# Kernel optimization log

Hardware: AMD Instinct MI355X
Metric: run time of the kernel (lower is better)

## Reference

```python
import jax, jax.numpy as jnp
import numpy as np

N, E = 100000, 3200000
F_NODE, F_EDGE = 2, 7
H, C = 4, 8
HC = H * C
REG, TGT = 500, 1
NUM_LAYERS = 3
ATT_SLOPE = 0.2   # LeakyReLU inside GATv2 attention
ACT_SLOPE = 0.01  # model-level LeakyReLU default
BN_EPS = 1e-5


def gatv2(x, src, dst, e_attr, Wl, bl, Wr, br, We, att, bias):
    n = x.shape[0]
    xl = (x @ Wl + bl).reshape(n, H, C)          # source transform (messages)
    xr = (x @ Wr + br).reshape(n, H, C)          # destination transform
    ee = (e_attr @ We).reshape(-1, H, C)         # edge transform (no bias in PyG)
    m = jax.nn.leaky_relu(xl[src] + xr[dst] + ee, ATT_SLOPE)  # [Ef,H,C]
    logits = jnp.einsum('ehc,hc->eh', m, att)    # [Ef,H]
    mx = jax.ops.segment_max(logits, dst, num_segments=n)
    ex = jnp.exp(logits - mx[dst])
    den = jax.ops.segment_sum(ex, dst, num_segments=n)
    alpha = ex / (den[dst] + 1e-16)              # edge-softmax grouped by dst
    out = jax.ops.segment_sum(xl[src] * alpha[:, :, None], dst, num_segments=n)
    return out.reshape(n, HC) + bias             # concat heads + bias


def setup_inputs() -> dict:
    key = jax.random.key(0)
    ks = jax.random.split(key, 30)
    # edges with no self loops (module calls add_self_loops on top)
    s = jax.random.randint(ks[0], (E,), 0, N, dtype=jnp.int32)
    off = jax.random.randint(ks[1], (E,), 1, N, dtype=jnp.int32)
    d = (s + off) % N
    edge_index = jnp.stack([s, d])
    x = jax.random.normal(ks[2], (N, F_NODE), dtype=jnp.float32)
    edge_attr = jax.random.normal(ks[3], (E, F_EDGE), dtype=jnp.float32)

    def glorot(k, shape):
        fan = shape[0] + shape[-1]
        return jax.random.normal(k, shape, dtype=jnp.float32) * jnp.sqrt(2.0 / fan)

    inp = dict(x=x, edge_index=edge_index, edge_attr=edge_attr)
    i = 4
    for tag, fin in (("1", F_NODE), ("2", HC)):
        inp["Wl" + tag] = glorot(ks[i], (fin, HC)); i += 1
        inp["bl" + tag] = jnp.zeros((HC,), jnp.float32)
        inp["Wr" + tag] = glorot(ks[i], (fin, HC)); i += 1
        inp["br" + tag] = jnp.zeros((HC,), jnp.float32)
        inp["We" + tag] = glorot(ks[i], (F_EDGE, HC)); i += 1
        inp["att" + tag] = glorot(ks[i], (H, C)); i += 1
        inp["b" + tag] = jnp.zeros((HC,), jnp.float32)
    inp["gamma"] = jnp.ones((HC,), jnp.float32)
    inp["beta"] = jnp.zeros((HC,), jnp.float32)
    inp["Wreg"] = glorot(ks[i], (HC, REG)); i += 1
    inp["breg"] = jnp.zeros((REG,), jnp.float32)
    inp["Wend"] = glorot(ks[i], (REG, TGT)); i += 1
    inp["bend"] = jnp.zeros((TGT,), jnp.float32)
    return inp


def reference(x, edge_index, edge_attr,
              Wl1, bl1, Wr1, br1, We1, att1, b1,
              Wl2, bl2, Wr2, br2, We2, att2, b2,
              gamma, beta, Wreg, breg, Wend, bend):
    n = x.shape[0]
    loop = jnp.arange(n, dtype=edge_index.dtype)
    srcf = jnp.concatenate([edge_index[0], loop])
    dstf = jnp.concatenate([edge_index[1], loop])
    # self-loop edge attrs filled with mean (PyG fill_value='mean')
    ea_mean = jnp.mean(edge_attr, axis=0, keepdims=True)
    eaf = jnp.concatenate([edge_attr, jnp.broadcast_to(ea_mean, (n, edge_attr.shape[1]))])

    h = gatv2(x, srcf, dstf, eaf, Wl1, bl1, Wr1, br1, We1, att1, b1)
    for _ in range(NUM_LAYERS - 1):
        mu = jnp.mean(h, axis=0)
        var = jnp.var(h, axis=0)
        h = (h - mu) * jax.lax.rsqrt(var + BN_EPS) * gamma + beta
        h = jax.nn.leaky_relu(h, ACT_SLOPE)
        h = gatv2(h, srcf, dstf, eaf, Wl2, bl2, Wr2, br2, We2, att2, b2)
    h = jax.nn.leaky_relu(h, ACT_SLOPE)
    h = h @ Wreg + breg
    return h @ Wend + bend
```

## Files before the change

### kernel.cpp

```cpp
#include <hip/hip_runtime.h>
#include <hip/hip_fp16.h>
#include <math.h>

#define NN 100000
#define EE 3200000
#define FE 7
#define GNB 32
#define CRR 1280
#define NBK 391
#define BKCAP 8688
#define T1 4096
#define FB1 ((EE + T1 - 1) / T1)

typedef unsigned int uivec4 __attribute__((ext_vector_type(4)));
static __device__ __forceinline__ uint4 ntload4(const uint4* p) {
    uivec4 v = __builtin_nontemporal_load((const uivec4*)p);
    uint4 r; r.x = v.x; r.y = v.y; r.z = v.z; r.w = v.w; return r;
}

static __device__ __forceinline__ __half2 hmax2(__half2 a, __half2 b) {
    unsigned int ua = *(unsigned int*)&a, ub = *(unsigned int*)&b, ur;
    asm("v_pk_max_f16 %0, %1, %2" : "=v"(ur) : "v"(ua), "v"(ub));
    return *(__half2*)&ur;
}


__global__ void k_prep(const float* __restrict__ Wreg, const float* __restrict__ breg,
                       const float* __restrict__ Wend, const float* __restrict__ bend,
                       float* __restrict__ wend, float* __restrict__ c0v,
                       int* __restrict__ gbucket) {
    if (blockIdx.x == 0) {
        int t = threadIdx.x;
        if (t < 32) {
            float s = 0.f;
            for (int k = 0; k < 500; ++k) s = fmaf(Wreg[t * 500 + k], Wend[k], s);
            wend[t] = s;
        } else if (t == 32) {
            float s = 0.f;
            for (int k = 0; k < 500; ++k) s = fmaf(breg[k], Wend[k], s);
            *c0v = s + bend[0];
        }
    } else {
        for (int i = threadIdx.x; i < NBK; i += 256) gbucket[i] = i * BKCAP;
    }
}

__global__ __launch_bounds__(512) void k_fill1(const int* __restrict__ ei,
                                               const float* __restrict__ ea,
                                               int* __restrict__ gbucket,
                                               uint4* __restrict__ srt,
                                               double* __restrict__ ea_sum) {
    __shared__ int hbin[NBK];
    __shared__ float part[8][FE];
    for (int i = threadIdx.x; i < NBK; i += 512) hbin[i] = 0;
    __syncthreads();
    int e0 = blockIdx.x * T1;
    int rb[8];
#pragma unroll
    for (int i = 0; i < 8; ++i) {
        int e = e0 + i * 512 + threadIdx.x;
        int v = -1;
        if (e < EE) {
            int d = __builtin_nontemporal_load(ei + EE + e);
            int b = d >> 8;
            int r = atomicAdd(&hbin[b], 1);
            v = (r << 17) | ((d & 255) << 9) | b;
        }
        rb[i] = v;
    }
    __syncthreads();
    for (int i = threadIdx.x; i < NBK; i += 512) {
        int c = hbin[i];
        hbin[i] = (c > 0) ? atomicAdd(&gbucket[i], c) : 0;
    }
    __syncthreads();
    float acc[FE];
#pragma unroll
    for (int f = 0; f < FE; ++f) acc[f] = 0.f;
#pragma unroll
    for (int i = 0; i < 8; ++i) {
        int v = rb[i];
        if (v < 0) continue;
        int e = e0 + i * 512 + threadIdx.x;
        int b = v & 511;
        unsigned dl = (unsigned)((v >> 9) & 255);
        int r = v >> 17;
        int pos = hbin[b] + r;
        int s = __builtin_nontemporal_load(ei + e);
        const float* rr = ea + (size_t)e * FE;
        unsigned h[FE];
#pragma unroll
        for (int f = 0; f < FE; ++f) {
            float af = __builtin_nontemporal_load(rr + f);
            acc[f] += af;
            h[f] = (unsigned)__half_as_ushort(__float2half_rn(af));
        }
#pragma unroll
        for (int f = 0; f < 6; ++f) { h[f] = (h[f] + 1) >> 1; if (h[f] > 0x7FFFu) h[f] = 0x7FFFu; }
        unsigned h6 = (h[6] + 4) >> 3; if (h6 > 0x1FFFu) h6 = 0x1FFFu;
        uint4 u;
        u.x = h[0] | (h[1] << 15) | ((dl & 3u) << 30);
        u.y = h[2] | (h[3] << 15) | (((dl >> 2) & 3u) << 30);
        u.z = h[4] | (h[5] << 15) | (((dl >> 4) & 3u) << 30);
        u.w = (unsigned)s | (h6 << 17) | ((dl >> 6) << 30);
        srt[(size_t)pos] = u;
    }
    int wave = threadIdx.x >> 6;
#pragma unroll
    for (int f = 0; f < FE; ++f) {
        float v = acc[f];
        for (int o = 32; o > 0; o >>= 1) v += __shfl_down(v, o, 64);
        if ((threadIdx.x & 63) == 0) part[wave][f] = v;
    }
    __syncthreads();
    if (threadIdx.x < FE) {
        float s = 0.f;
#pragma unroll
        for (int i = 0; i < 8; ++i) s += part[i][threadIdx.x];
        atomicAdd(&ea_sum[threadIdx.x], (double)s);
    }
}

__global__ __launch_bounds__(512) void k_bscan(const int* __restrict__ gbucket,
                                               int* __restrict__ bbase,
                                               const double* __restrict__ ea_sum,
                                               float* __restrict__ ea_mean) {
    __shared__ int ts[512];
    int t = threadIdx.x;
    if (t < 8) ea_mean[t] = (t < FE) ? (float)(ea_sum[t] / (double)EE) : 0.f;
    int c = (t < NBK) ? (gbucket[t] - t * BKCAP) : 0;
    ts[t] = c;
    __syncthreads();
    for (int o = 1; o < 512; o <<= 1) {
        int u = (t >= o) ? ts[t - o] : 0;
        __syncthreads();
        ts[t] += u;
        __syncthreads();
    }
    if (t < NBK) bbase[t] = ts[t] - c;
}

__global__ __launch_bounds__(512) void k_fill2(const uint4* __restrict__ srt,
                                               const int* __restrict__ gbucket,
                                               const int* __restrict__ bbase,
                                               int* __restrict__ offs,
                                               uint4* __restrict__ rec) {
    __shared__ int hist[256], hcopy[256], strt[256];
    int t = threadIdx.x;
    int b = blockIdx.x;
    int nbase = b << 8;
    int nb = NN - nbase; if (nb > 256) nb = 256;
    int sbase = b * BKCAP;
    int cnt = gbucket[b] - sbase;
    int bb = bbase[b];
    if (t < 256) hist[t] = 0;
    __syncthreads();
    for (int p = t; p < cnt; p += 512) {
        uint4 s = srt[(size_t)(sbase + p)];
        int dl = (int)((s.x >> 30) | ((s.y >> 30) << 2) | ((s.z >> 30) << 4) | ((s.w >> 30) << 6));
        atomicAdd(&hist[dl], 1);
    }
    __syncthreads();
    if (t < 256) hcopy[t] = hist[t];
    __syncthreads();
    for (int o = 1; o < 256; o <<= 1) {
        int u = 0;
        if (t < 256 && t >= o) u = hist[t - o];
        __syncthreads();
        if (t < 256) hist[t] += u;
        __syncthreads();
    }
    if (t < 256) {
        int c = hcopy[t];
        int start = bb + hist[t] - c;
        strt[t] = start;
        if (t < nb) offs[nbase + t] = start + c;
    }
    __syncthreads();
    for (int p = t; p < cnt; p += 512) {
        uint4 s = srt[(size_t)(sbase + p)];
        int dl = (int)((s.x >> 30) | ((s.y >> 30) << 2) | ((s.z >> 30) << 4) | ((s.w >> 30) << 6));
        int pos = atomicAdd(&strt[dl], 1);
        uint4 u;
        u.x = ((s.x & 0x7FFFu) << 1) | (((s.x >> 15) & 0x7FFFu) << 17);
        u.y = ((s.y & 0x7FFFu) << 1) | (((s.y >> 15) & 0x7FFFu) << 17);
        u.z = ((s.z & 0x7FFFu) << 1) | (((s.z >> 15) & 0x7FFFu) << 17);
        u.w = (s.w & 0x1FFFFu) | (((s.w >> 17) & 0x1FFFu) << 19);
        rec[(size_t)pos] = u;
    }
}

template <int FIN, bool BN>
__global__ void k_xform(const float* __restrict__ h,
                        const float* __restrict__ Wl, const float* __restrict__ bl,
                        const float* __restrict__ Wr, const float* __restrict__ br,
                        const double* __restrict__ bn_part, const double* __restrict__ bn_sqpart,
                        const float* __restrict__ gamma, const float* __restrict__ beta,
                        __half* __restrict__ xl, __half* __restrict__ xr) {
    __shared__ float sWl[FIN * 32], sWr[FIN * 32], sb[64];
    __shared__ float smu[FIN], ssc[FIN], sbe[FIN];
    for (int i = threadIdx.x; i < FIN * 32; i += blockDim.x) { sWl[i] = Wl[i]; sWr[i] = Wr[i]; }
    if (threadIdx.x < 32) { sb[threadIdx.x] = bl[threadIdx.x]; sb[32 + threadIdx.x] = br[threadIdx.x]; }
    if (BN && threadIdx.x < FIN) {
        int f = threadIdx.x;
        double s = 0.0, q = 0.0;
#pragma unroll
        for (int k = 0; k < 32; ++k) { s += bn_part[k * 32 + f]; q += bn_sqpart[k * 32 + f]; }
        double mu = s * (1.0 / NN);
        double var = q * (1.0 / NN) - mu * mu;
        smu[f] = (float)mu;
        ssc[f] = gamma[f] * (float)(1.0 / sqrt(var + 1e-5));
        sbe[f] = beta[f];
    }
    __syncthreads();
    int idx = blockIdx.x * blockDim.x + threadIdx.x;
    if (idx >= NN * 32) return;
    int n = idx >> 5, c = idx & 31;
    const float* hr = h + (size_t)n * FIN;
    float al = sb[c], ar = sb[32 + c];
#pragma unroll
    for (int f = 0; f < FIN; ++f) {
        float v = hr[f];
        if (BN) {
            v = fmaf(v - smu[f], ssc[f], sbe[f]);
            v = v > 0.f ? v : 0.01f * v;
        }
        al = fmaf(v, sWl[f * 32 + c], al);
        ar = fmaf(v, sWr[f * 32 + c], ar);
    }
    xl[idx] = __float2half(al);
    xr[idx] = __float2half(ar);
}

template <int MODE>
__global__ __launch_bounds__(256) void k_gat_t(
    const int* __restrict__ offs, const uint4* __restrict__ rec,
    const __half* __restrict__ xl, const __half* __restrict__ xr,
    const float* __restrict__ We, const float* __restrict__ att,
    const float* __restrict__ bias, const float* __restrict__ ea_mean,
    float* __restrict__ hout, double* __restrict__ bn_part,
    double* __restrict__ bn_sqpart, const float* __restrict__ wend,
    const float* __restrict__ c0v, float* __restrict__ out) {
    __shared__ uint4 srec[CRR];
    int n0 = blockIdx.x * GNB;
    int g = threadIdx.x >> 3, j = threadIdx.x & 7, c0 = j * 4;
    int node = n0 + g;

    __half2 weh[FE][2];
#pragma unroll
    for (int f = 0; f < FE; ++f) {
        weh[f][0] = __floats2half2_rn(We[f * 32 + c0], We[f * 32 + c0 + 1]);
        weh[f][1] = __floats2half2_rn(We[f * 32 + c0 + 2], We[f * 32 + c0 + 3]);
    }
    float at0 = att[c0], at1 = att[c0 + 1], at2 = att[c0 + 2], at3 = att[c0 + 3];
    float eam[FE];
#pragma unroll
    for (int f = 0; f < FE; ++f) eam[f] = ea_mean[f];

    float2 rawr = *(const float2*)(xr + (size_t)node * 32 + c0);
    __half2 qh01 = *(const __half2*)&rawr.x;
    __half2 qh23 = *(const __half2*)&rawr.y;
    float2 q01 = __half22float2(qh01);
    float2 q23 = __half22float2(qh23);

    int s_g = (node == 0) ? 0 : offs[node - 1];
    int e_g = offs[node];
    int range0 = (n0 == 0) ? 0 : offs[n0 - 1];
    int range1 = offs[n0 + GNB - 1];

    float sm = 0.f, acc0 = 0.f, acc1 = 0.f, acc2 = 0.f, acc3 = 0.f;
    const __half2 c02 = __float2half2_rn(0.2f);

    auto edge_op = [&](uint4 u, float2 rawl) {
        __half2 lh01 = *(const __half2*)&rawl.x;
        __half2 lh23 = *(const __half2*)&rawl.y;
        __half2 ah01 = *(const __half2*)&u.x;
        __half2 ah23 = *(const __half2*)&u.y;
        __half2 ah45 = *(const __half2*)&u.z;
        __half a6h = __ushort_as_half((unsigned short)((u.w >> 16) & 0xFFFEu));
        __half2 e01 = qh01, e23 = qh23;
        __half2 bc;
        bc = __low2half2(ah01);  e01 = __hfma2(bc, weh[0][0], e01); e23 = __hfma2(bc, weh[0][1], e23);
        bc = __high2half2(ah01); e01 = __hfma2(bc, weh[1][0], e01); e23 = __hfma2(bc, weh[1][1], e23);
        bc = __low2half2(ah23);  e01 = __hfma2(bc, weh[2][0], e01); e23 = __hfma2(bc, weh[2][1], e23);
        bc = __high2half2(ah23); e01 = __hfma2(bc, weh[3][0], e01); e23 = __hfma2(bc, weh[3][1], e23);
        bc = __low2half2(ah45);  e01 = __hfma2(bc, weh[4][0], e01); e23 = __hfma2(bc, weh[4][1], e23);
        bc = __high2half2(ah45); e01 = __hfma2(bc, weh[5][0], e01); e23 = __hfma2(bc, weh[5][1], e23);
        bc = __half2half2(a6h);  e01 = __hfma2(bc, weh[6][0], e01); e23 = __hfma2(bc, weh[6][1], e23);
        __half2 v01 = __hadd2(e01, lh01);
        __half2 v23 = __hadd2(e23, lh23);
        v01 = hmax2(v01, __hmul2(v01, c02));
        v23 = hmax2(v23, __hmul2(v23, c02));
        float2 f01 = __half22float2(v01), f23 = __half22float2(v23);
        float pl = fmaf(f01.x, at0, fmaf(f01.y, at1, fmaf(f23.x, at2, f23.y * at3)));
        float L = pl + __shfl_xor(pl, 1, 64);
        float ex = __expf(L);
        sm += ex;
        float2 l01 = __half22float2(lh01), l23 = __half22float2(lh23);
        acc0 = fmaf(ex, l01.x, acc0);
        acc1 = fmaf(ex, l01.y, acc1);
        acc2 = fmaf(ex, l23.x, acc2);
        acc3 = fmaf(ex, l23.y, acc3);
    };

    for (int base = range0; base < range1; base += CRR) {
        int cnt = range1 - base; if (cnt > CRR) cnt = CRR;
        __syncthreads();
        for (int i = threadIdx.x; i < cnt; i += 256)
            srec[i] = ntload4(&rec[(size_t)base + i]);
        __syncthreads();
        int lo = s_g > base ? s_g : base;
        int hi = e_g < base + cnt ? e_g : base + cnt;
        if (lo >= hi) continue;
        int i1 = lo + 1 < hi ? lo + 1 : hi - 1;
        int i2 = lo + 2 < hi ? lo + 2 : hi - 1;
        uint4 ua = srec[lo - base];
        float2 ra = *(const float2*)(xl + (size_t)(ua.w & 0x1FFFFu) * 32 + c0);
        uint4 ub = srec[i1 - base];
        float2 rb = *(const float2*)(xl + (size_t)(ub.w & 0x1FFFFu) * 32 + c0);
        uint4 uc = srec[i2 - base];
        float2 rc = *(const float2*)(xl + (size_t)(uc.w & 0x1FFFFu) * 32 + c0);
#pragma unroll 3
        for (int p = lo; p < hi; ++p) {
            uint4 cu = ua; float2 cr = ra;
            ua = ub; ra = rb;
            ub = uc; rb = rc;
            int pn = p + 3 < hi ? p + 3 : hi - 1;
            uc = srec[pn - base];
            rc = *(const float2*)(xl + (size_t)(uc.w & 0x1FFFFu) * 32 + c0);
            edge_op(cu, cr);
        }
    }

    {
        float2 rawl = *(const float2*)(xl + (size_t)node * 32 + c0);
        float2 l01 = __half22float2(*(const __half2*)&rawl.x);
        float2 l23 = __half22float2(*(const __half2*)&rawl.y);
        float ee0 = q01.x, ee1 = q01.y, ee2 = q23.x, ee3 = q23.y;
        float wef[FE][4];
#pragma unroll
        for (int f = 0; f < FE; ++f) {
            float2 w0 = __half22float2(weh[f][0]);
            float2 w1 = __half22float2(weh[f][1]);
            wef[f][0] = w0.x; wef[f][1] = w0.y; wef[f][2] = w1.x; wef[f][3] = w1.y;
        }
#pragma unroll
        for (int f = 0; f < FE; ++f) {
            ee0 = fmaf(eam[f], wef[f][0], ee0);
            ee1 = fmaf(eam[f], wef[f][1], ee1);
            ee2 = fmaf(eam[f], wef[f][2], ee2);
            ee3 = fmaf(eam[f], wef[f][3], ee3);
        }
        float v0 = ee0 + l01.x;
        float v1 = ee1 + l01.y;
        float v2 = ee2 + l23.x;
        float v3 = ee3 + l23.y;
        v0 = fmaxf(v0, 0.2f * v0);
        v1 = fmaxf(v1, 0.2f * v1);
        v2 = fmaxf(v2, 0.2f * v2);
        v3 = fmaxf(v3, 0.2f * v3);
        float pl = fmaf(v0, at0, fmaf(v1, at1, fmaf(v2, at2, v3 * at3)));
        float L = pl + __shfl_xor(pl, 1, 64);
        float ex = __expf(L);
        sm += ex;
        acc0 = fmaf(ex, l01.x, acc0);
        acc1 = fmaf(ex, l01.y, acc1);
        acc2 = fmaf(ex, l23.x, acc2);
        acc3 = fmaf(ex, l23.y, acc3);
    }

    float inv = 1.f / (sm + 1e-16f);
    float o0 = fmaf(acc0, inv, bias[c0 + 0]);
    float o1 = fmaf(acc1, inv, bias[c0 + 1]);
    float o2 = fmaf(acc2, inv, bias[c0 + 2]);
    float o3 = fmaf(acc3, inv, bias[c0 + 3]);
    if constexpr (MODE != 2) {
        float4 o; o.x = o0; o.y = o1; o.z = o2; o.w = o3;
        *(float4*)(hout + (size_t)node * 32 + c0) = o;
    }
    if constexpr (MODE == 1) {
        float s0 = o0, s1 = o1, s2 = o2, s3 = o3;
        float z0 = o0 * o0, z1 = o1 * o1, z2 = o2 * o2, z3 = o3 * o3;
#pragma unroll
        for (int off = 8; off < 64; off <<= 1) {
            s0 += __shfl_xor(s0, off, 64); z0 += __shfl_xor(z0, off, 64);
            s1 += __shfl_xor(s1, off, 64); z1 += __shfl_xor(z1, off, 64);
            s2 += __shfl_xor(s2, off, 64); z2 += __shfl_xor(z2, off, 64);
            s3 += __shfl_xor(s3, off, 64); z3 += __shfl_xor(z3, off, 64);
        }
        __syncthreads();
        float* red = (float*)srec;
        int wv = threadIdx.x >> 6, lane = threadIdx.x & 63;
        if (lane < 8) {
            float* r = red + (wv * 8 + lane) * 8;
            r[0] = s0; r[1] = s1; r[2] = s2; r[3] = s3;
            r[4] = z0; r[5] = z1; r[6] = z2; r[7] = z3;
        }
        __syncthreads();
        if (threadIdx.x < 32) {
            int jj = threadIdx.x >> 2, kk = threadIdx.x & 3;
            float ts = 0.f, tq = 0.f;
#pragma unroll
            for (int w2 = 0; w2 < 4; ++w2) {
                ts += red[(w2 * 8 + jj) * 8 + kk];
                tq += red[(w2 * 8 + jj) * 8 + 4 + kk];
            }
            int slot = (blockIdx.x & 31) * 32 + threadIdx.x;
            atomicAdd(&bn_part[slot], (double)ts);
            atomicAdd(&bn_sqpart[slot], (double)tq);
        }
    }
    if constexpr (MODE == 2) {
        float w0 = wend[c0], w1 = wend[c0 + 1], w2 = wend[c0 + 2], w3 = wend[c0 + 3];
        float p0 = o0 > 0.f ? o0 : 0.01f * o0;
        float p1 = o1 > 0.f ? o1 : 0.01f * o1;
        float p2 = o2 > 0.f ? o2 : 0.01f * o2;
        float p3 = o3 > 0.f ? o3 : 0.01f * o3;
        float p = fmaf(p0, w0, fmaf(p1, w1, fmaf(p2, w2, p3 * w3)));
        p += __shfl_xor(p, 1, 64);
        p += __shfl_xor(p, 2, 64);
        p += __shfl_xor(p, 4, 64);
        if (j == 0) out[node] = p + *c0v;
    }
}

extern "C" void kernel_launch(void* const* d_in, const int* in_sizes, int n_in,
                              void* d_out, int out_size, void* d_ws, size_t ws_size,
                              hipStream_t stream) {
    (void)in_sizes; (void)n_in; (void)out_size; (void)ws_size;
    const float* x    = (const float*)d_in[0];
    const int*   ei   = (const int*)d_in[1];
    const float* ea   = (const float*)d_in[2];
    const float* Wl1  = (const float*)d_in[3];
    const float* bl1  = (const float*)d_in[4];
    const float* Wr1  = (const float*)d_in[5];
    const float* br1  = (const float*)d_in[6];
    const float* We1  = (const float*)d_in[7];
    const float* att1 = (const float*)d_in[8];
    const float* b1   = (const float*)d_in[9];
    const float* Wl2  = (const float*)d_in[10];
    const float* bl2  = (const float*)d_in[11];
    const float* Wr2  = (const float*)d_in[12];
    const float* br2  = (const float*)d_in[13];
    const float* We2  = (const float*)d_in[14];
    const float* att2 = (const float*)d_in[15];
    const float* b2   = (const float*)d_in[16];
    const float* gamma= (const float*)d_in[17];
    const float* beta = (const float*)d_in[18];
    const float* Wreg = (const float*)d_in[19];
    const float* breg = (const float*)d_in[20];
    const float* Wend = (const float*)d_in[21];
    const float* bend = (const float*)d_in[22];
    float* out = (float*)d_out;

    char* w = (char*)d_ws;
    double* ea_sum   = (double*)(w + 0);
    float*  ea_mean  = (float*)(w + 576);
    float*  wend     = (float*)(w + 608);
    float*  c0v      = (float*)(w + 736);
    int*    gbucket  = (int*)(w + 2048);
    int*    bbase    = (int*)(w + 4096);
    double* bn_part  = (double*)(w + 8192);
    double* bn_sqp   = (double*)(w + 16384);
    size_t o = 24576;
    int* offs = (int*)(w + o); o += ((size_t)NN * 4 + 255) & ~(size_t)255;
    __half* xl = (__half*)(w + o); o += ((size_t)NN * 32 * 2 + 255) & ~(size_t)255;
    __half* xr = (__half*)(w + o); o += ((size_t)NN * 32 * 2 + 255) & ~(size_t)255;
    float* hb = (float*)(w + o); o += (size_t)NN * 32 * 4;
    uint4* rec = (uint4*)(w + o); o += (size_t)EE * 16;
    uint4* srt = (uint4*)(w + o); o += (size_t)NBK * BKCAP * 16;

    hipMemsetAsync(w, 0, 1024, stream);
    hipMemsetAsync(w + 8192, 0, 16384, stream);

    k_prep<<<2, 256, 0, stream>>>(Wreg, breg, Wend, bend, wend, c0v, gbucket);
    k_fill1<<<FB1, 512, 0, stream>>>(ei, ea, gbucket, srt, ea_sum);
    k_bscan<<<1, 512, 0, stream>>>(gbucket, bbase, ea_sum, ea_mean);
    k_fill2<<<NBK, 512, 0, stream>>>(srt, gbucket, bbase, offs, rec);

    const int xbl = (NN * 32 + 255) / 256;
    const int gbl = NN / GNB;

    k_xform<2, false><<<xbl, 256, 0, stream>>>(x, Wl1, bl1, Wr1, br1,
                                               bn_part, bn_sqp, gamma, beta, xl, xr);
    k_gat_t<1><<<gbl, 256, 0, stream>>>(offs, rec, xl, xr, We1, att1, b1, ea_mean,
                                        hb, bn_part, bn_sqp, wend, c0v, out);

    k_xform<32, true><<<xbl, 256, 0, stream>>>(hb, Wl2, bl2, Wr2, br2,
                                               bn_part, bn_sqp, gamma, beta, xl, xr);
    hipMemsetAsync(w + 8192, 0, 16384, stream);
    k_gat_t<1><<<gbl, 256, 0, stream>>>(offs, rec, xl, xr, We2, att2, b2, ea_mean,
                                        hb, bn_part, bn_sqp, wend, c0v, out);

    k_xform<32, true><<<xbl, 256, 0, stream>>>(hb, Wl2, bl2, Wr2, br2,
                                               bn_part, bn_sqp, gamma, beta, xl, xr);
    k_gat_t<2><<<gbl, 256, 0, stream>>>(offs, rec, xl, xr, We2, att2, b2, ea_mean,
                                        hb, bn_part, bn_sqp, wend, c0v, out);
}
```

Baseline: 673.3 us.

## Double fill tile size and reserve bucket slots with a second atomic pass

Each k_fill1 block now handles 8192 edges instead of 4096, which halves the number of blocks and the global atomics on bucket counters. The per-edge rank is no longer packed into registers. A first loop only histograms destinations, and a second loop re-reads the destination index and claims its slot with a shared atomicAdd on the bucket base. The trade is a second read of the dst indices, twice as many shared atomics, and non-contiguous loops that are no longer unrolled.

```diff
diff --git a/kernel.cpp b/kernel.cpp
--- a/kernel.cpp
+++ b/kernel.cpp
@@ -9,7 +9,7 @@
 #define CRR 1280
 #define NBK 391
 #define BKCAP 8688
-#define T1 4096
+#define T1 8192
 #define FB1 ((EE + T1 - 1) / T1)
 
 typedef unsigned int uivec4 __attribute__((ext_vector_type(4)));
@@ -55,18 +55,10 @@
     for (int i = threadIdx.x; i < NBK; i += 512) hbin[i] = 0;
     __syncthreads();
     int e0 = blockIdx.x * T1;
-    int rb[8];
-#pragma unroll
-    for (int i = 0; i < 8; ++i) {
-        int e = e0 + i * 512 + threadIdx.x;
-        int v = -1;
-        if (e < EE) {
-            int d = __builtin_nontemporal_load(ei + EE + e);
-            int b = d >> 8;
-            int r = atomicAdd(&hbin[b], 1);
-            v = (r << 17) | ((d & 255) << 9) | b;
-        }
-        rb[i] = v;
+    int ecnt = EE - e0; if (ecnt > T1) ecnt = T1;
+    for (int i = threadIdx.x; i < ecnt; i += 512) {
+        int d = ei[EE + e0 + i];
+        atomicAdd(&hbin[d >> 8], 1);
     }
     __syncthreads();
     for (int i = threadIdx.x; i < NBK; i += 512) {
@@ -77,16 +69,13 @@
     float acc[FE];
 #pragma unroll
     for (int f = 0; f < FE; ++f) acc[f] = 0.f;
-#pragma unroll
-    for (int i = 0; i < 8; ++i) {
-        int v = rb[i];
-        if (v < 0) continue;
-        int e = e0 + i * 512 + threadIdx.x;
-        int b = v & 511;
-        unsigned dl = (unsigned)((v >> 9) & 255);
-        int r = v >> 17;
-        int pos = hbin[b] + r;
-        int s = __builtin_nontemporal_load(ei + e);
+    for (int i = threadIdx.x; i < ecnt; i += 512) {
+        int e = e0 + i;
+        int d = ei[EE + e];
+        int b = d >> 8;
+        unsigned dl = (unsigned)(d & 255);
+        int pos = atomicAdd(&hbin[b], 1);
+        int s = ei[e];
         const float* rr = ea + (size_t)e * FE;
         unsigned h[FE];
 #pragma unroll
```

New measurement: 671.7 us. About the same (-0.2%).
